# Kernel optimization log

Measured on AMD Instinct MI355X. Metric: run time of the kernel, lower is better.

## Reference

```python
import jax, jax.numpy as jnp
import numpy as np

N_NODES = 50000
N_EDGES = 800000
IN_DIM = 128
HIDDEN = 128
N_CLASSES = 10
BN_EPS = 1e-5


def _sage_conv(x, src, dst, n, w_l, b_l, w_r):
    # PyG SAGEConv (mean aggr): out = lin_l(mean_{j->i} x_j) + lin_r(x_i)
    msg = x[src]  # [E, d] gather
    s = jax.ops.segment_sum(msg, dst, num_segments=n)
    cnt = jax.ops.segment_sum(jnp.ones((src.shape[0], 1), x.dtype), dst, num_segments=n)
    mean = s / jnp.maximum(cnt, 1.0)
    return mean @ w_l.T + b_l + x @ w_r.T


def _bn_eval(x, gamma, beta, mean, var):
    return (x - mean) * (gamma * jax.lax.rsqrt(var + BN_EPS)) + beta


def setup_inputs() -> dict:
    key = jax.random.key(0)
    ks = jax.random.split(key, 16)
    h2 = HIDDEN // 2

    def lin(k, fan_out, fan_in):
        bound = 1.0 / np.sqrt(fan_in)
        return jax.random.uniform(k, (fan_out, fan_in), jnp.float32, -bound, bound)

    return {
        "x": jax.random.normal(ks[0], (N_NODES, IN_DIM), jnp.float32),
        "edge_index": jax.random.randint(ks[1], (2, N_EDGES), 0, N_NODES, jnp.int64),
        "w1l": lin(ks[2], HIDDEN, IN_DIM),
        "b1l": jnp.zeros((HIDDEN,), jnp.float32),
        "w1r": lin(ks[3], HIDDEN, IN_DIM),
        "bn1_gamma": jax.random.uniform(ks[4], (HIDDEN,), jnp.float32, 0.5, 1.5),
        "bn1_beta": jax.random.normal(ks[5], (HIDDEN,), jnp.float32) * 0.1,
        "bn1_mean": jax.random.normal(ks[6], (HIDDEN,), jnp.float32) * 0.1,
        "bn1_var": jax.random.uniform(ks[7], (HIDDEN,), jnp.float32, 0.5, 1.5),
        "w2l": lin(ks[8], h2, HIDDEN),
        "b2l": jnp.zeros((h2,), jnp.float32),
        "w2r": lin(ks[9], h2, HIDDEN),
        "bn2_gamma": jax.random.uniform(ks[10], (h2,), jnp.float32, 0.5, 1.5),
        "bn2_beta": jax.random.normal(ks[11], (h2,), jnp.float32) * 0.1,
        "bn2_mean": jax.random.normal(ks[12], (h2,), jnp.float32) * 0.1,
        "bn2_var": jax.random.uniform(ks[13], (h2,), jnp.float32, 0.5, 1.5),
        "head_w": lin(ks[14], N_CLASSES, h2),
        "head_b": jnp.zeros((N_CLASSES,), jnp.float32),
    }


def reference(x, edge_index, w1l, b1l, w1r, bn1_gamma, bn1_beta, bn1_mean, bn1_var,
              w2l, b2l, w2r, bn2_gamma, bn2_beta, bn2_mean, bn2_var, head_w, head_b):
    src, dst = edge_index[0], edge_index[1]
    n = x.shape[0]
    h = _sage_conv(x, src, dst, n, w1l, b1l, w1r)
    h = jax.nn.relu(_bn_eval(h, bn1_gamma, bn1_beta, bn1_mean, bn1_var))
    # dropout p=0.1 is identity in eval mode
    h = _sage_conv(h, src, dst, n, w2l, b2l, w2r)
    h = jax.nn.relu(_bn_eval(h, bn2_gamma, bn2_beta, bn2_mean, bn2_var))
    return h @ head_w.T + head_b
```

## Files before the change

### kernel.cpp

```cpp
#include <hip/hip_runtime.h>

typedef _Float16 f16;
typedef _Float16 f16x2 __attribute__((ext_vector_type(2)));
typedef _Float16 f16x8 __attribute__((ext_vector_type(8)));
typedef float f32x4 __attribute__((ext_vector_type(4)));

#define N_NODES 50000
#define N_EDGES 800000
#define N_CLASSES 10
#define CAP 64
#define EDGE_BLOCKS ((N_EDGES + 255) / 256)
#define XCVT_BLOCKS (N_NODES * 128 / 8 / 256)

__global__ void zero_cnt_kernel(int* __restrict__ cnt) {
    int i = blockIdx.x * 256 + threadIdx.x;
    if (i < N_NODES / 4) ((int4*)cnt)[i] = make_int4(0, 0, 0, 0);
}

__global__ void build_fused_kernel(const int* __restrict__ src, const int* __restrict__ dst,
                                   int* __restrict__ cnt, unsigned short* __restrict__ bucket,
                                   const float* __restrict__ x,
                                   const float* __restrict__ w1l, const float* __restrict__ w1r,
                                   const float* __restrict__ w2l, const float* __restrict__ w2r,
                                   f16* __restrict__ xh, f16* __restrict__ W1, f16* __restrict__ W2) {
    int bid = blockIdx.x;
    if (bid < 2 * EDGE_BLOCKS) {
        int half = bid >> 1;
        if ((bid & 1) == 0) {
            int e = half * 256 + threadIdx.x;
            if (e < N_EDGES) {
                int d = dst[e];
                int s = atomicAdd(&cnt[d], 1);
                if (s < CAP) bucket[(long long)d * CAP + s] = (unsigned short)src[e];
            }
        } else {
            long long base = ((long long)half * 256 + threadIdx.x) * 8;
            float4 a = *(const float4*)(x + base);
            float4 b = *(const float4*)(x + base + 4);
            f16x8 o;
            o[0] = (f16)a.x; o[1] = (f16)a.y; o[2] = (f16)a.z; o[3] = (f16)a.w;
            o[4] = (f16)b.x; o[5] = (f16)b.y; o[6] = (f16)b.z; o[7] = (f16)b.w;
            *(f16x8*)(xh + base) = o;
        }
    } else {
        int wt = (bid - 2 * EDGE_BLOCKS) * 256 + threadIdx.x;
        for (int idx = wt; idx < 128 * 256; idx += 1024) {
            int n = idx >> 8, k = idx & 255;
            W1[idx] = (f16)(k < 128 ? w1l[n * 128 + k] : w1r[n * 128 + k - 128]);
        }
        for (int idx = wt; idx < 64 * 256; idx += 1024) {
            int n = idx >> 8, k = idx & 255;
            W2[idx] = (f16)(k < 128 ? w2l[n * 128 + k] : w2r[n * 128 + k - 128]);
        }
    }
}

__global__ void agg_mean_f16_kernel(const f16* __restrict__ feat,
                                    const int* __restrict__ cnt,
                                    const unsigned short* __restrict__ bucket,
                                    f16* __restrict__ outb) {
    int node = blockIdx.x * 4 + (threadIdx.x >> 6);
    int lane = threadIdx.x & 63;
    if (node >= N_NODES) return;
    int deg = cnt[node];
    int n_it = deg < CAP ? deg : CAP;
    const unsigned short* b = bucket + (long long)node * CAP;
    int myidx = (lane < n_it) ? (int)b[lane] : 0;
    const f16x2* f2 = (const f16x2*)feat;
    float ax = 0.f, ay = 0.f;
    int j = 0;
    for (; j + 8 <= n_it; j += 8) {
        f16x2 v0 = f2[(long long)__shfl(myidx, j + 0) * 64 + lane];
        f16x2 v1 = f2[(long long)__shfl(myidx, j + 1) * 64 + lane];
        f16x2 v2 = f2[(long long)__shfl(myidx, j + 2) * 64 + lane];
        f16x2 v3 = f2[(long long)__shfl(myidx, j + 3) * 64 + lane];
        f16x2 v4 = f2[(long long)__shfl(myidx, j + 4) * 64 + lane];
        f16x2 v5 = f2[(long long)__shfl(myidx, j + 5) * 64 + lane];
        f16x2 v6 = f2[(long long)__shfl(myidx, j + 6) * 64 + lane];
        f16x2 v7 = f2[(long long)__shfl(myidx, j + 7) * 64 + lane];
        ax += (((float)v0[0] + (float)v1[0]) + ((float)v2[0] + (float)v3[0]))
            + (((float)v4[0] + (float)v5[0]) + ((float)v6[0] + (float)v7[0]));
        ay += (((float)v0[1] + (float)v1[1]) + ((float)v2[1] + (float)v3[1]))
            + (((float)v4[1] + (float)v5[1]) + ((float)v6[1] + (float)v7[1]));
    }
    for (; j + 4 <= n_it; j += 4) {
        f16x2 v0 = f2[(long long)__shfl(myidx, j + 0) * 64 + lane];
        f16x2 v1 = f2[(long long)__shfl(myidx, j + 1) * 64 + lane];
        f16x2 v2 = f2[(long long)__shfl(myidx, j + 2) * 64 + lane];
        f16x2 v3 = f2[(long long)__shfl(myidx, j + 3) * 64 + lane];
        ax += ((float)v0[0] + (float)v1[0]) + ((float)v2[0] + (float)v3[0]);
        ay += ((float)v0[1] + (float)v1[1]) + ((float)v2[1] + (float)v3[1]);
    }
    for (; j < n_it; j++) {
        f16x2 v = f2[(long long)__shfl(myidx, j) * 64 + lane];
        ax += (float)v[0];
        ay += (float)v[1];
    }
    float inv = 1.f / fmaxf((float)deg, 1.f);
    f16x2 r;
    r[0] = (f16)(ax * inv);
    r[1] = (f16)(ay * inv);
    ((f16x2*)outb)[(long long)node * 64 + lane] = r;
}

template<int NOUT, bool FUSE_HEAD>
__global__ __launch_bounds__(256) void sage_mfma_kernel(
    const f16* __restrict__ Am,
    const f16* __restrict__ Ax,
    const f16* __restrict__ W,
    const float* __restrict__ bias,
    const float* __restrict__ gamma,
    const float* __restrict__ beta,
    const float* __restrict__ bmean,
    const float* __restrict__ bvar,
    f16* __restrict__ C,
    const float* __restrict__ hw,
    const float* __restrict__ hb,
    float* __restrict__ outp)
{
    constexpr int NF = NOUT / 16;
    __shared__ f16 smem[FUSE_HEAD ? 128 : 1][FUSE_HEAD ? 68 : 1];

    int tid  = threadIdx.x;
    int wave = tid >> 6;
    int lane = tid & 63;
    int m_base = blockIdx.x * 128 + wave * 32;
    int lrow = lane & 15;
    int lchunk = lane >> 4;

    f32x4 acc[2][NF] = {};

#pragma unroll
    for (int phase = 0; phase < 2; phase++) {
        const f16* A = phase ? Ax : Am;
        const f16* Wp = W + phase * 128;

        f16x8 afrag[4][2];
#pragma unroll
        for (int kc = 0; kc < 4; kc++)
#pragma unroll
            for (int mf = 0; mf < 2; mf++) {
                int row = m_base + mf * 16 + lrow;
                row = row < N_NODES ? row : N_NODES - 1;
                afrag[kc][mf] = *(const f16x8*)(A + (long long)row * 128 + kc * 32 + lchunk * 8);
            }

#pragma unroll
        for (int nf = 0; nf < NF; nf++) {
#pragma unroll
            for (int kc = 0; kc < 4; kc++) {
                f16x8 b = *(const f16x8*)(Wp + (long long)(nf * 16 + lrow) * 256
                                          + kc * 32 + lchunk * 8);
                acc[0][nf] = __builtin_amdgcn_mfma_f32_16x16x32_f16(afrag[kc][0], b, acc[0][nf], 0, 0, 0);
                acc[1][nf] = __builtin_amdgcn_mfma_f32_16x16x32_f16(afrag[kc][1], b, acc[1][nf], 0, 0, 0);
            }
        }
    }

#pragma unroll
    for (int nf = 0; nf < NF; nf++) {
        int n = nf * 16 + lrow;
        float mul = gamma[n] * rsqrtf(bvar[n] + 1e-5f);
        float add = (bias[n] - bmean[n]) * mul + beta[n];
#pragma unroll
        for (int mf = 0; mf < 2; mf++) {
#pragma unroll
            for (int r = 0; r < 4; r++) {
                int mloc = wave * 32 + mf * 16 + lchunk * 4 + r;
                float v = fmaxf(fmaf(acc[mf][nf][r], mul, add), 0.f);
                if (FUSE_HEAD) {
                    smem[mloc][n] = (f16)v;
                } else {
                    int m = blockIdx.x * 128 + mloc;
                    if (m < N_NODES) C[(long long)m * NOUT + n] = (f16)v;
                }
            }
        }
    }

    if (FUSE_HEAD) {
        __syncthreads();
        int rl = tid >> 1;
        int m = blockIdx.x * 128 + rl;
        int cb = (tid & 1) * 5;
        if (m < N_NODES) {
            float a0 = hb[cb + 0], a1 = hb[cb + 1], a2 = hb[cb + 2];
            float a3 = hb[cb + 3], a4 = hb[cb + 4];
#pragma unroll 8
            for (int k = 0; k < 64; k++) {
                float hv = (float)smem[rl][k];
                a0 = fmaf(hv, hw[(cb + 0) * 64 + k], a0);
                a1 = fmaf(hv, hw[(cb + 1) * 64 + k], a1);
                a2 = fmaf(hv, hw[(cb + 2) * 64 + k], a2);
                a3 = fmaf(hv, hw[(cb + 3) * 64 + k], a3);
                a4 = fmaf(hv, hw[(cb + 4) * 64 + k], a4);
            }
            float* op = outp + (long long)m * N_CLASSES + cb;
            op[0] = a0; op[1] = a1; op[2] = a2; op[3] = a3; op[4] = a4;
        }
    }
}

extern "C" void kernel_launch(void* const* d_in, const int* in_sizes, int n_in,
                              void* d_out, int out_size, void* d_ws, size_t ws_size,
                              hipStream_t stream) {
    const float* x      = (const float*)d_in[0];
    const int*   ei     = (const int*)d_in[1];
    const float* w1l    = (const float*)d_in[2];
    const float* b1l    = (const float*)d_in[3];
    const float* w1r    = (const float*)d_in[4];
    const float* bn1_g  = (const float*)d_in[5];
    const float* bn1_b  = (const float*)d_in[6];
    const float* bn1_m  = (const float*)d_in[7];
    const float* bn1_v  = (const float*)d_in[8];
    const float* w2l    = (const float*)d_in[9];
    const float* b2l    = (const float*)d_in[10];
    const float* w2r    = (const float*)d_in[11];
    const float* bn2_g  = (const float*)d_in[12];
    const float* bn2_b  = (const float*)d_in[13];
    const float* bn2_m  = (const float*)d_in[14];
    const float* bn2_v  = (const float*)d_in[15];
    const float* head_w = (const float*)d_in[16];
    const float* head_b = (const float*)d_in[17];
    float* out = (float*)d_out;

    const int* src  = ei;
    const int* dstv = ei + N_EDGES;

    char* ws = (char*)d_ws;
    size_t off = 0;
    int* cnt               = (int*)(ws + off); off += ((size_t)N_NODES * 4 + 511) & ~511ull;
    unsigned short* bucket = (unsigned short*)(ws + off); off += (size_t)N_NODES * CAP * 2;
    f16* xh      = (f16*)(ws + off); off += (size_t)N_NODES * 128 * 2;
    f16* meanb   = (f16*)(ws + off); off += (size_t)N_NODES * 128 * 2;
    f16* h1      = (f16*)(ws + off); off += (size_t)N_NODES * 128 * 2;
    f16* W1      = (f16*)(ws + off); off += (size_t)128 * 256 * 2;
    f16* W2      = (f16*)(ws + off); off += (size_t)64 * 256 * 2;

    zero_cnt_kernel<<<(N_NODES / 4 + 255) / 256, 256, 0, stream>>>(cnt);
    build_fused_kernel<<<2 * EDGE_BLOCKS + 4, 256, 0, stream>>>(
        src, dstv, cnt, bucket, x, w1l, w1r, w2l, w2r, xh, W1, W2);

    agg_mean_f16_kernel<<<(N_NODES + 3) / 4, 256, 0, stream>>>(xh, cnt, bucket, meanb);
    sage_mfma_kernel<128, false><<<(N_NODES + 127) / 128, 256, 0, stream>>>(
        meanb, xh, W1, b1l, bn1_g, bn1_b, bn1_m, bn1_v, h1, nullptr, nullptr, nullptr);

    agg_mean_f16_kernel<<<(N_NODES + 3) / 4, 256, 0, stream>>>(h1, cnt, bucket, meanb);
    sage_mfma_kernel<64, true><<<(N_NODES + 127) / 128, 256, 0, stream>>>(
        meanb, h1, W2, b2l, bn2_g, bn2_b, bn2_m, bn2_v, nullptr, head_w, head_b, out);
}
```

Before: 154.2 us.

## Project layer-2 features before aggregation to halve gather width

Uses linearity of mean aggregation: layer-2 weights (w2l and w2r concatenated) are applied to h1 inside the layer-1 MFMA kernel, producing a 128-wide y2. The second aggregation then gathers only the 64-wide w2l projection, and a new final kernel adds the w2r half, applies BN/ReLU and the head. This halves the bytes moved by the second neighbour gather and drops the separate h1 round-trip, at the cost of an extra y2/mean2 buffer, an extra launch and different fp16 rounding order.

```diff
diff --git a/kernel.cpp b/kernel.cpp
--- a/kernel.cpp
+++ b/kernel.cpp
@@ -22,7 +22,7 @@
                                    const float* __restrict__ x,
                                    const float* __restrict__ w1l, const float* __restrict__ w1r,
                                    const float* __restrict__ w2l, const float* __restrict__ w2r,
-                                   f16* __restrict__ xh, f16* __restrict__ W1, f16* __restrict__ W2) {
+                                   f16* __restrict__ xh, f16* __restrict__ W1, f16* __restrict__ W2cat) {
     int bid = blockIdx.x;
     if (bid < 2 * EDGE_BLOCKS) {
         int half = bid >> 1;
@@ -48,9 +48,9 @@
             int n = idx >> 8, k = idx & 255;
             W1[idx] = (f16)(k < 128 ? w1l[n * 128 + k] : w1r[n * 128 + k - 128]);
         }
-        for (int idx = wt; idx < 64 * 256; idx += 1024) {
-            int n = idx >> 8, k = idx & 255;
-            W2[idx] = (f16)(k < 128 ? w2l[n * 128 + k] : w2r[n * 128 + k - 128]);
+        for (int idx = wt; idx < 128 * 128; idx += 1024) {
+            int n = idx >> 7, k = idx & 127;
+            W2cat[idx] = (f16)(n < 64 ? w2l[n * 128 + k] : w2r[(n - 64) * 128 + k]);
         }
     }
 }
@@ -103,23 +103,19 @@
     ((f16x2*)outb)[(long long)node * 64 + lane] = r;
 }
 
-template<int NOUT, bool FUSE_HEAD>
-__global__ __launch_bounds__(256) void sage_mfma_kernel(
+__global__ __launch_bounds__(256) void sage1_y2_kernel(
     const f16* __restrict__ Am,
     const f16* __restrict__ Ax,
-    const f16* __restrict__ W,
+    const f16* __restrict__ W1,
     const float* __restrict__ bias,
     const float* __restrict__ gamma,
     const float* __restrict__ beta,
     const float* __restrict__ bmean,
     const float* __restrict__ bvar,
-    f16* __restrict__ C,
-    const float* __restrict__ hw,
-    const float* __restrict__ hb,
-    float* __restrict__ outp)
+    const f16* __restrict__ W2cat,
+    f16* __restrict__ y2)
 {
-    constexpr int NF = NOUT / 16;
-    __shared__ f16 smem[FUSE_HEAD ? 128 : 1][FUSE_HEAD ? 68 : 1];
+    __shared__ f16 ldsA[4][32][136];
 
     int tid  = threadIdx.x;
     int wave = tid >> 6;
@@ -128,12 +124,12 @@
     int lrow = lane & 15;
     int lchunk = lane >> 4;
 
-    f32x4 acc[2][NF] = {};
+    f32x4 acc[2][8] = {};
 
 #pragma unroll
     for (int phase = 0; phase < 2; phase++) {
         const f16* A = phase ? Ax : Am;
-        const f16* Wp = W + phase * 128;
+        const f16* Wp = W1 + phase * 128;
 
         f16x8 afrag[4][2];
 #pragma unroll
@@ -146,7 +142,7 @@
             }
 
 #pragma unroll
-        for (int nf = 0; nf < NF; nf++) {
+        for (int nf = 0; nf < 8; nf++) {
 #pragma unroll
             for (int kc = 0; kc < 4; kc++) {
                 f16x8 b = *(const f16x8*)(Wp + (long long)(nf * 16 + lrow) * 256
@@ -158,7 +154,7 @@
     }
 
 #pragma unroll
-    for (int nf = 0; nf < NF; nf++) {
+    for (int nf = 0; nf < 8; nf++) {
         int n = nf * 16 + lrow;
         float mul = gamma[n] * rsqrtf(bvar[n] + 1e-5f);
         float add = (bias[n] - bmean[n]) * mul + beta[n];
@@ -166,38 +162,112 @@
         for (int mf = 0; mf < 2; mf++) {
 #pragma unroll
             for (int r = 0; r < 4; r++) {
-                int mloc = wave * 32 + mf * 16 + lchunk * 4 + r;
-                float v = fmaxf(fmaf(acc[mf][nf][r], mul, add), 0.f);
-                if (FUSE_HEAD) {
-                    smem[mloc][n] = (f16)v;
-                } else {
-                    int m = blockIdx.x * 128 + mloc;
-                    if (m < N_NODES) C[(long long)m * NOUT + n] = (f16)v;
-                }
-            }
-        }
-    }
-
-    if (FUSE_HEAD) {
-        __syncthreads();
-        int rl = tid >> 1;
-        int m = blockIdx.x * 128 + rl;
-        int cb = (tid & 1) * 5;
-        if (m < N_NODES) {
-            float a0 = hb[cb + 0], a1 = hb[cb + 1], a2 = hb[cb + 2];
-            float a3 = hb[cb + 3], a4 = hb[cb + 4];
+                int rloc = mf * 16 + lchunk * 4 + r;
+                ldsA[wave][rloc][n] = (f16)fmaxf(fmaf(acc[mf][nf][r], mul, add), 0.f);
+            }
+        }
+    }
+
+#pragma unroll
+    for (int nf2 = 0; nf2 < 8; nf2++) {
+        f32x4 acc2[2] = {};
+#pragma unroll
+        for (int kc = 0; kc < 4; kc++) {
+            f16x8 b2 = *(const f16x8*)(W2cat + (long long)(nf2 * 16 + lrow) * 128
+                                       + kc * 32 + lchunk * 8);
+            f16x8 a0 = *(const f16x8*)&ldsA[wave][lrow][kc * 32 + lchunk * 8];
+            f16x8 a1 = *(const f16x8*)&ldsA[wave][16 + lrow][kc * 32 + lchunk * 8];
+            acc2[0] = __builtin_amdgcn_mfma_f32_16x16x32_f16(a0, b2, acc2[0], 0, 0, 0);
+            acc2[1] = __builtin_amdgcn_mfma_f32_16x16x32_f16(a1, b2, acc2[1], 0, 0, 0);
+        }
+        int n = nf2 * 16 + lrow;
+#pragma unroll
+        for (int mf = 0; mf < 2; mf++) {
+#pragma unroll
+            for (int r = 0; r < 4; r++) {
+                int m = m_base + mf * 16 + lchunk * 4 + r;
+                if (m < N_NODES) y2[(long long)m * 128 + n] = (f16)acc2[mf][r];
+            }
+        }
+    }
+}
+
+__global__ void agg_half_kernel(const f16* __restrict__ y2,
+                                const int* __restrict__ cnt,
+                                const unsigned short* __restrict__ bucket,
+                                f16* __restrict__ mean2) {
+    int node = blockIdx.x * 4 + (threadIdx.x >> 6);
+    int lane = threadIdx.x & 63;
+    if (node >= N_NODES) return;
+    int deg = cnt[node];
+    int n_it = deg < CAP ? deg : CAP;
+    const unsigned short* b = bucket + (long long)node * CAP;
+    int myidx = (lane < n_it) ? (int)b[lane] : 0;
+    float a = 0.f;
+    int j = 0;
+    for (; j + 8 <= n_it; j += 8) {
+        float t0 = (float)y2[(long long)__shfl(myidx, j + 0) * 128 + lane];
+        float t1 = (float)y2[(long long)__shfl(myidx, j + 1) * 128 + lane];
+        float t2 = (float)y2[(long long)__shfl(myidx, j + 2) * 128 + lane];
+        float t3 = (float)y2[(long long)__shfl(myidx, j + 3) * 128 + lane];
+        float t4 = (float)y2[(long long)__shfl(myidx, j + 4) * 128 + lane];
+        float t5 = (float)y2[(long long)__shfl(myidx, j + 5) * 128 + lane];
+        float t6 = (float)y2[(long long)__shfl(myidx, j + 6) * 128 + lane];
+        float t7 = (float)y2[(long long)__shfl(myidx, j + 7) * 128 + lane];
+        a += ((t0 + t1) + (t2 + t3)) + ((t4 + t5) + (t6 + t7));
+    }
+    for (; j < n_it; j++)
+        a += (float)y2[(long long)__shfl(myidx, j) * 128 + lane];
+    mean2[(long long)node * 64 + lane] = (f16)(a / fmaxf((float)deg, 1.f));
+}
+
+__global__ void final_head_kernel(const f16* __restrict__ mean2,
+                                  const f16* __restrict__ y2,
+                                  const float* __restrict__ b2,
+                                  const float* __restrict__ gamma,
+                                  const float* __restrict__ beta,
+                                  const float* __restrict__ bmean,
+                                  const float* __restrict__ bvar,
+                                  const float* __restrict__ hw,
+                                  const float* __restrict__ hb,
+                                  float* __restrict__ outp) {
+    __shared__ f16 sm[128][68];
+    int t = threadIdx.x;
+    int rl = t >> 1, hh = t & 1;
+    int m = blockIdx.x * 128 + rl;
+    if (m < N_NODES) {
+        int ch0 = hh * 32;
+#pragma unroll
+        for (int c = 0; c < 32; c += 8) {
+            int ch = ch0 + c;
+            f16x8 mv = *(const f16x8*)(mean2 + (long long)m * 64 + ch);
+            f16x8 yv = *(const f16x8*)(y2 + (long long)m * 128 + 64 + ch);
+#pragma unroll
+            for (int i = 0; i < 8; i++) {
+                int n = ch + i;
+                float mul = gamma[n] * rsqrtf(bvar[n] + 1e-5f);
+                float add = (b2[n] - bmean[n]) * mul + beta[n];
+                float v = fmaf((float)mv[i] + (float)yv[i], mul, add);
+                sm[rl][n] = (f16)fmaxf(v, 0.f);
+            }
+        }
+    }
+    __syncthreads();
+    if (m < N_NODES) {
+        int cb = hh * 5;
+        float a0 = hb[cb + 0], a1 = hb[cb + 1], a2 = hb[cb + 2];
+        float a3 = hb[cb + 3], a4 = hb[cb + 4];
 #pragma unroll 8
-            for (int k = 0; k < 64; k++) {
-                float hv = (float)smem[rl][k];
-                a0 = fmaf(hv, hw[(cb + 0) * 64 + k], a0);
-                a1 = fmaf(hv, hw[(cb + 1) * 64 + k], a1);
-                a2 = fmaf(hv, hw[(cb + 2) * 64 + k], a2);
-                a3 = fmaf(hv, hw[(cb + 3) * 64 + k], a3);
-                a4 = fmaf(hv, hw[(cb + 4) * 64 + k], a4);
-            }
-            float* op = outp + (long long)m * N_CLASSES + cb;
-            op[0] = a0; op[1] = a1; op[2] = a2; op[3] = a3; op[4] = a4;
-        }
+        for (int k = 0; k < 64; k++) {
+            float hv = (float)sm[rl][k];
+            a0 = fmaf(hv, hw[(cb + 0) * 64 + k], a0);
+            a1 = fmaf(hv, hw[(cb + 1) * 64 + k], a1);
+            a2 = fmaf(hv, hw[(cb + 2) * 64 + k], a2);
+            a3 = fmaf(hv, hw[(cb + 3) * 64 + k], a3);
+            a4 = fmaf(hv, hw[(cb + 4) * 64 + k], a4);
+        }
+        float* op = outp + (long long)m * N_CLASSES + cb;
+        op[0] = a0; op[1] = a1; op[2] = a2; op[3] = a3; op[4] = a4;
     }
 }
 
@@ -231,21 +301,22 @@
     size_t off = 0;
     int* cnt               = (int*)(ws + off); off += ((size_t)N_NODES * 4 + 511) & ~511ull;
     unsigned short* bucket = (unsigned short*)(ws + off); off += (size_t)N_NODES * CAP * 2;
-    f16* xh      = (f16*)(ws + off); off += (size_t)N_NODES * 128 * 2;
-    f16* meanb   = (f16*)(ws + off); off += (size_t)N_NODES * 128 * 2;
-    f16* h1      = (f16*)(ws + off); off += (size_t)N_NODES * 128 * 2;
-    f16* W1      = (f16*)(ws + off); off += (size_t)128 * 256 * 2;
-    f16* W2      = (f16*)(ws + off); off += (size_t)64 * 256 * 2;
+    f16* xh     = (f16*)(ws + off); off += (size_t)N_NODES * 128 * 2;
+    f16* meanb  = (f16*)(ws + off); off += (size_t)N_NODES * 128 * 2;
+    f16* y2     = (f16*)(ws + off); off += (size_t)N_NODES * 128 * 2;
+    f16* mean2  = (f16*)(ws + off); off += (size_t)N_NODES * 64 * 2;
+    f16* W1     = (f16*)(ws + off); off += (size_t)128 * 256 * 2;
+    f16* W2cat  = (f16*)(ws + off); off += (size_t)128 * 128 * 2;
 
     zero_cnt_kernel<<<(N_NODES / 4 + 255) / 256, 256, 0, stream>>>(cnt);
     build_fused_kernel<<<2 * EDGE_BLOCKS + 4, 256, 0, stream>>>(
-        src, dstv, cnt, bucket, x, w1l, w1r, w2l, w2r, xh, W1, W2);
+        src, dstv, cnt, bucket, x, w1l, w1r, w2l, w2r, xh, W1, W2cat);
 
     agg_mean_f16_kernel<<<(N_NODES + 3) / 4, 256, 0, stream>>>(xh, cnt, bucket, meanb);
-    sage_mfma_kernel<128, false><<<(N_NODES + 127) / 128, 256, 0, stream>>>(
-        meanb, xh, W1, b1l, bn1_g, bn1_b, bn1_m, bn1_v, h1, nullptr, nullptr, nullptr);
-
-    agg_mean_f16_kernel<<<(N_NODES + 3) / 4, 256, 0, stream>>>(h1, cnt, bucket, meanb);
-    sage_mfma_kernel<64, true><<<(N_NODES + 127) / 128, 256, 0, stream>>>(
-        meanb, h1, W2, b2l, bn2_g, bn2_b, bn2_m, bn2_v, nullptr, head_w, head_b, out);
-}
+    sage1_y2_kernel<<<(N_NODES + 127) / 128, 256, 0, stream>>>(
+        meanb, xh, W1, b1l, bn1_g, bn1_b, bn1_m, bn1_v, W2cat, y2);
+
+    agg_half_kernel<<<(N_NODES + 3) / 4, 256, 0, stream>>>(y2, cnt, bucket, mean2);
+    final_head_kernel<<<(N_NODES + 127) / 128, 256, 0, stream>>>(
+        mean2, y2, b2l, bn2_g, bn2_b, bn2_m, bn2_v, head_w, head_b, out);
+}
```

New measurement: 158.7 us. 2.9% more time.
